# Kernel tuning notes

Hardware: AMD Instinct MI355X
Metric: run time of the kernel (lower is better)

The kernel has to match this reference:

```python
import jax, jax.numpy as jnp
import numpy as np

D_MODEL = 64  # per-head dim used in the scale sqrt(d_model*2)
B, H, S, D = 4, 16, 2048, 64


def setup_inputs() -> dict:
    key = jax.random.key(0)
    kq, kk, kv, kd, ke, km = jax.random.split(key, 6)
    return {
        "Q": jax.random.normal(kq, (B, H, S, D), dtype=jnp.float32),
        "K": jax.random.normal(kk, (B, H, S, D), dtype=jnp.float32),
        "V": jax.random.normal(kv, (B, H, S, D), dtype=jnp.float32),
        "distance_matrix": jax.random.uniform(kd, (B, S, S), dtype=jnp.float32),
        "energy_matrix": jax.random.uniform(ke, (B, S, S), dtype=jnp.float32),
        "mask": jax.random.randint(km, (B, 1, S, S), 0, 2, dtype=jnp.int32),
    }


def reference(Q, K, V, distance_matrix, energy_matrix, mask):
    # distance_matrix and energy_matrix are unused by the original forward.
    scale = 1.0 / np.sqrt(D_MODEL * 2).astype(np.float32)
    scores = jnp.einsum("bhqd,bhkd->bhqk", Q, K) * scale  # [B,H,S,S]
    scores = jnp.where(mask == 0, jnp.float32(-1e9), scores)
    attn = jax.nn.softmax(scores, axis=-1)
    context = jnp.einsum("bhqk,bhkd->bhqd", attn, V)  # [B,H,S,D]
    return context
```

## Files before the change

kernel.cpp:

```cpp
#include <hip/hip_runtime.h>
#include <stdint.h>

#define DEVINL __device__ __forceinline__

typedef float f32x4 __attribute__((ext_vector_type(4)));
typedef float f32x2 __attribute__((ext_vector_type(2)));
typedef short s16x8 __attribute__((ext_vector_type(8)));
typedef short s16x4 __attribute__((ext_vector_type(4)));
typedef unsigned int u32x4 __attribute__((ext_vector_type(4)));

constexpr int Bb = 4, Hh = 16, Ss = 2048, Dd = 64;
constexpr float SCALE = 0.088388347648318447f;
constexpr float QSC = 0.088388347648318447f * 1.4426950408889634f;

DEVINL short f2bf(float x) {
  union { float f; unsigned u; } c; c.f = x;
  unsigned r = (c.u + 0x7fffu + ((c.u >> 16) & 1u)) >> 16;
  return (short)r;
}

DEVINL unsigned pkbf(float a, float b) {
  unsigned r;
  asm("v_cvt_pk_bf16_f32 %0, %1, %2" : "=v"(r) : "v"(a), "v"(b));
  return r;
}

DEVINL void gload_lds16(const short* g, short* l) {
  __builtin_amdgcn_global_load_lds(
      (const __attribute__((address_space(1))) void*)g,
      (__attribute__((address_space(3))) void*)l, 16, 0, 0);
}

__global__ void mask_to_bits(const int* __restrict__ mask,
                             unsigned long long* __restrict__ bits, int n) {
  int gid = blockIdx.x * blockDim.x + threadIdx.x;
  int stride = gridDim.x * blockDim.x;
  for (int i = gid; i < n; i += stride) {
    unsigned long long bal = __ballot(mask[i] != 0);
    if ((i & 63) == 0) bits[i >> 6] = bal;
  }
}

__global__ void kvconv(const float* __restrict__ K, const float* __restrict__ V,
                       short* __restrict__ Kimg, short* __restrict__ Vimg) {
  const int x = blockIdx.x;
  const int sel = x & 1;
  const int t = (x >> 1) & 31;
  const int bh = x >> 6;
  const int tid = threadIdx.x;
  if (sel == 0) {
    const float* Kp = K + ((size_t)bh * Ss + t * 64) * Dd;
    short* img = Kimg + ((size_t)bh * 32 + t) * 4096;
#pragma unroll
    for (int it = 0; it < 4; ++it) {
      int idx = tid + it * 256;
      int kv = idx >> 4, c = idx & 15;
      const float* kr = Kp + (size_t)kv * Dd;
      s16x4 sv;
      sv[0] = f2bf(kr[c]);
      sv[1] = f2bf(kr[c + 16]);
      sv[2] = f2bf(kr[c + 32]);
      sv[3] = f2bf(kr[c + 48]);
      *(s16x4*)(img + kv * 64 + ((4 * c) ^ ((kv & 7) << 3))) = sv;
    }
  } else {
    const float* Vp = V + ((size_t)bh * Ss + t * 64) * Dd;
    short* img = Vimg + ((size_t)bh * 32 + t) * 4096;
    const int d = tid & 63, c4 = tid >> 6;
#pragma unroll
    for (int it = 0; it < 4; ++it) {
      int c = c4 * 4 + it;
      s16x4 sv;
      sv[0] = f2bf(Vp[(size_t)(c) * Dd + d]);
      sv[1] = f2bf(Vp[(size_t)(c + 16) * Dd + d]);
      sv[2] = f2bf(Vp[(size_t)(c + 32) * Dd + d]);
      sv[3] = f2bf(Vp[(size_t)(c + 48) * Dd + d]);
      *(s16x4*)(img + d * 64 + ((4 * c) ^ ((d & 7) << 3))) = sv;
    }
  }
}

__launch_bounds__(256, 5)
__global__ void attn2(const float* __restrict__ Q,
                      const unsigned long long* __restrict__ mbits,
                      const short* __restrict__ Kimg,
                      const short* __restrict__ Vimg,
                      float* __restrict__ Out) {
  __shared__ short lds[16384];

  const int tid = threadIdx.x;
  const int lane = tid & 63;
  const int w = tid >> 6;
  const int l15 = lane & 15;
  const int lq = lane >> 4;

  const int nb = ((blockIdx.x & 7) << 8) | (blockIdx.x >> 3);
  const int qt = nb & 31;
  const int bh = nb >> 5;
  const int b = bh >> 4;

  const float* Qp = Q + (size_t)bh * Ss * Dd;
  float* Op = Out + (size_t)bh * Ss * Dd;
  const short* Kt = Kimg + (size_t)bh * 32 * 4096;
  const short* Vt = Vimg + (size_t)bh * 32 * 4096;
  const int qbW = qt * 64 + w * 16;

  s16x8 qf[2];
  {
    const float* qrow = Qp + (size_t)(qbW + l15) * Dd;
#pragma unroll
    for (int dh = 0; dh < 2; ++dh) {
      s16x8 f;
#pragma unroll
      for (int g = 0; g < 4; ++g) {
        f32x2 v = *(const f32x2*)(qrow + 16 * g + 4 * lq + 2 * dh);
        f[g] = f2bf(v[0] * QSC);
        f[g + 4] = f2bf(v[1] * QSC);
      }
      qf[dh] = f;
    }
  }

  s16x8 onesA;
  {
    short o = (l15 == 0) ? (short)0x3F80 : (short)0;
#pragma unroll
    for (int j = 0; j < 8; ++j) onesA[j] = o;
  }

  f32x4 oacc[4];
  f32x4 lacc = f32x4{0.f, 0.f, 0.f, 0.f};
#pragma unroll
  for (int ds = 0; ds < 4; ++ds) oacc[ds] = f32x4{0.f, 0.f, 0.f, 0.f};

  int off[4][2];
#pragma unroll
  for (int sub = 0; sub < 4; ++sub) {
    int row = sub * 16 + l15;
    int sw = (row & 7) << 3;
    off[sub][0] = row * 64 + ((16 * lq) ^ sw);
    off[sub][1] = row * 64 + ((16 * lq + 8) ^ sw);
  }

  const unsigned long long* mbq = mbits + (size_t)(b * Ss + qbW + l15) * 32;

  auto stage = [&](int buf, int t) {
    short* Lb = lds + buf * 8192;
    const short* gk = Kt + t * 4096 + w * 512 + lane * 8;
    const short* gv = Vt + t * 4096 + w * 512 + lane * 8;
    gload_lds16(gk, Lb + w * 512);
    gload_lds16(gk + 2048, Lb + 2048 + w * 512);
    gload_lds16(gv, Lb + 4096 + w * 512);
    gload_lds16(gv + 2048, Lb + 6144 + w * 512);
  };

  stage(0, 0);

  for (int t = 0; t < 32; ++t) {
    const int cur = t & 1;
    unsigned long long mw = mbq[t];
    __syncthreads();
    if (t < 31) stage(cur ^ 1, t + 1);

    const short* kb = lds + cur * 8192;
    const short* vb = kb + 4096;

    f32x4 bias[4];
    {
      const unsigned mlo = ~(unsigned)(mw >> (4 * lq));
      const unsigned mhi = ~(unsigned)(mw >> (32 + 4 * lq));
#pragma unroll
      for (int sub = 0; sub < 4; ++sub) {
        const unsigned wsrc = (sub < 2) ? mlo : mhi;
        const int base = 16 * (sub & 1);
#pragma unroll
        for (int r = 0; r < 4; ++r) {
          int sb = ((int)(wsrc << (31 - (base + r)))) >> 31;
          bias[sub][r] = __uint_as_float((unsigned)sb & 0xCE6E6B28u);
        }
      }
    }

    f32x4 sc[4];
    __builtin_amdgcn_s_setprio(1);
#pragma unroll
    for (int sub = 0; sub < 4; ++sub) {
      s16x8 k0 = *(const s16x8*)(kb + off[sub][0]);
      s16x8 k1 = *(const s16x8*)(kb + off[sub][1]);
      f32x4 a = bias[sub];
      a = __builtin_amdgcn_mfma_f32_16x16x32_bf16(k0, qf[0], a, 0, 0, 0);
      a = __builtin_amdgcn_mfma_f32_16x16x32_bf16(k1, qf[1], a, 0, 0, 0);
      sc[sub] = a;
    }
    __builtin_amdgcn_s_setprio(0);

    s16x8 pf[2];
#pragma unroll
    for (int sub = 0; sub < 4; ++sub) {
      f32x4 s = sc[sub];
#pragma unroll
      for (int r = 0; r < 4; ++r) s[r] = __builtin_amdgcn_exp2f(s[r]);
      sc[sub] = s;
    }
#pragma unroll
    for (int kvh = 0; kvh < 2; ++kvh) {
      u32x4 wv;
      wv[0] = pkbf(sc[0][2 * kvh], sc[1][2 * kvh]);
      wv[1] = pkbf(sc[2][2 * kvh], sc[3][2 * kvh]);
      wv[2] = pkbf(sc[0][2 * kvh + 1], sc[1][2 * kvh + 1]);
      wv[3] = pkbf(sc[2][2 * kvh + 1], sc[3][2 * kvh + 1]);
      pf[kvh] = __builtin_bit_cast(s16x8, wv);
    }

    __builtin_amdgcn_s_setprio(1);
#pragma unroll
    for (int ds = 0; ds < 4; ++ds) {
      s16x8 v0 = *(const s16x8*)(vb + off[ds][0]);
      s16x8 v1 = *(const s16x8*)(vb + off[ds][1]);
      f32x4 a = oacc[ds];
      a = __builtin_amdgcn_mfma_f32_16x16x32_bf16(v0, pf[0], a, 0, 0, 0);
      a = __builtin_amdgcn_mfma_f32_16x16x32_bf16(v1, pf[1], a, 0, 0, 0);
      oacc[ds] = a;
    }
    lacc = __builtin_amdgcn_mfma_f32_16x16x32_bf16(onesA, pf[0], lacc, 0, 0, 0);
    lacc = __builtin_amdgcn_mfma_f32_16x16x32_bf16(onesA, pf[1], lacc, 0, 0, 0);
    __builtin_amdgcn_s_setprio(0);
  }

  {
    float l = __shfl(lacc[0], l15);
    float inv = 1.f / l;
    float* orow = Op + (size_t)(qbW + l15) * Dd;
#pragma unroll
    for (int ds = 0; ds < 4; ++ds) {
      f32x4 v = oacc[ds];
      v *= inv;
      *(f32x4*)(orow + ds * 16 + 4 * lq) = v;
    }
  }
}

template<bool USEBITS>
__launch_bounds__(256, 2)
__global__ void attn_fwd(const float* __restrict__ Q, const float* __restrict__ K,
                         const float* __restrict__ V, const int* __restrict__ mask,
                         const unsigned long long* __restrict__ mbits,
                         float* __restrict__ Out) {
  __shared__ short Ks[64 * 64];
  __shared__ short Vs[64 * 64];

  const int tid = threadIdx.x;
  const int lane = tid & 63;
  const int w = tid >> 6;
  const int l15 = lane & 15;
  const int lq = lane >> 4;

  const int bid = blockIdx.x;
  const int h = bid & 15;
  const int qt = (bid >> 4) & 7;
  const int b = bid >> 7;

  const int bh = b * Hh + h;
  const float* Qp = Q + (size_t)bh * Ss * Dd;
  const float* Kp = K + (size_t)bh * Ss * Dd;
  const float* Vp = V + (size_t)bh * Ss * Dd;
  float* Op = Out + (size_t)bh * Ss * Dd;

  const int qbW = qt * 256 + w * 64;

  s16x8 qf[4][2];
#pragma unroll
  for (int qs = 0; qs < 4; ++qs) {
    const float* qrow = Qp + (size_t)(qbW + qs * 16 + l15) * Dd;
#pragma unroll
    for (int dh = 0; dh < 2; ++dh) {
      s16x8 f;
#pragma unroll
      for (int g = 0; g < 4; ++g) {
        f32x2 v = *(const f32x2*)(qrow + 16 * g + 4 * lq + 2 * dh);
        f[g] = f2bf(v[0]);
        f[g + 4] = f2bf(v[1]);
      }
      qf[qs][dh] = f;
    }
  }

  f32x4 oacc[4][4];
  float mrun[4], lrun[4];
#pragma unroll
  for (int qs = 0; qs < 4; ++qs) {
    mrun[qs] = -1e30f;
    lrun[qs] = 0.f;
#pragma unroll
    for (int ds = 0; ds < 4; ++ds) oacc[qs][ds] = f32x4{0.f, 0.f, 0.f, 0.f};
  }

  for (int kv0 = 0; kv0 < Ss; kv0 += 64) {
    __syncthreads();
#pragma unroll
    for (int p = 0; p < 4; ++p) {
      int f = tid + p * 256;
      int kv = f >> 4;
      int c = f & 15;
      const float* krow = Kp + (size_t)(kv0 + kv) * Dd;
      s16x4 sv;
      sv[0] = f2bf(krow[c]);
      sv[1] = f2bf(krow[c + 16]);
      sv[2] = f2bf(krow[c + 32]);
      sv[3] = f2bf(krow[c + 48]);
      *(s16x4*)(Ks + kv * 64 + ((4 * c) ^ ((kv & 7) << 3))) = sv;
    }
#pragma unroll
    for (int p = 0; p < 4; ++p) {
      int f = tid + p * 256;
      int kv = f >> 4;
      int c = f & 15;
      f32x4 v = *(const f32x4*)(Vp + (size_t)(kv0 + kv) * Dd + 4 * c);
      int pv = (kv & 15) * 4 + (kv >> 4);
#pragma unroll
      for (int i = 0; i < 4; ++i) {
        int d = 4 * c + i;
        Vs[d * 64 + (pv ^ ((d & 7) << 3))] = f2bf(v[i]);
      }
    }
    __syncthreads();

    s16x8 kf[4][2];
#pragma unroll
    for (int sub = 0; sub < 4; ++sub) {
      int row = sub * 16 + l15;
      const short* base = Ks + row * 64;
      int sw = (row & 7) << 3;
      kf[sub][0] = *(const s16x8*)(base + ((16 * lq + 0) ^ sw));
      kf[sub][1] = *(const s16x8*)(base + ((16 * lq + 8) ^ sw));
    }
    s16x8 vf[4][2];
#pragma unroll
    for (int ds = 0; ds < 4; ++ds) {
      int row = ds * 16 + l15;
      const short* base = Vs + row * 64;
      int sw = (row & 7) << 3;
      vf[ds][0] = *(const s16x8*)(base + ((16 * lq + 0) ^ sw));
      vf[ds][1] = *(const s16x8*)(base + ((16 * lq + 8) ^ sw));
    }

    const int kvw = kv0 >> 6;
#pragma unroll
    for (int qs = 0; qs < 4; ++qs) {
      f32x4 sc[4];
#pragma unroll
      for (int sub = 0; sub < 4; ++sub) {
        f32x4 a = f32x4{0.f, 0.f, 0.f, 0.f};
        a = __builtin_amdgcn_mfma_f32_16x16x32_bf16(kf[sub][0], qf[qs][0], a, 0, 0, 0);
        a = __builtin_amdgcn_mfma_f32_16x16x32_bf16(kf[sub][1], qf[qs][1], a, 0, 0, 0);
        sc[sub] = a;
      }

      const int q = qbW + qs * 16 + l15;
      unsigned long long mw = 0;
      if constexpr (USEBITS) mw = mbits[(size_t)(b * Ss + q) * 32 + kvw];

      float tm = -3e38f;
#pragma unroll
      for (int sub = 0; sub < 4; ++sub) {
        f32x4 s = sc[sub];
        if constexpr (USEBITS) {
          unsigned nib = (unsigned)((mw >> (16 * sub + 4 * lq)) & 0xFULL);
#pragma unroll
          for (int r = 0; r < 4; ++r) {
            float sv = s[r] * SCALE;
            sv = ((nib >> r) & 1u) ? sv : -1e9f;
            s[r] = sv;
            tm = fmaxf(tm, sv);
          }
        } else {
          const int* mrow = mask + ((size_t)b * Ss + q) * Ss + kv0 + 16 * sub + 4 * lq;
          int4 mi = *(const int4*)mrow;
          int mv[4] = {mi.x, mi.y, mi.z, mi.w};
#pragma unroll
          for (int r = 0; r < 4; ++r) {
            float sv = s[r] * SCALE;
            sv = mv[r] ? sv : -1e9f;
            s[r] = sv;
            tm = fmaxf(tm, sv);
          }
        }
        sc[sub] = s;
      }
      tm = fmaxf(tm, __shfl_xor(tm, 16));
      tm = fmaxf(tm, __shfl_xor(tm, 32));
      float mnew = fmaxf(mrun[qs], tm);
      float corr = __expf(mrun[qs] - mnew);
      mrun[qs] = mnew;

      float ps = 0.f;
#pragma unroll
      for (int sub = 0; sub < 4; ++sub) {
        f32x4 s = sc[sub];
#pragma unroll
        for (int r = 0; r < 4; ++r) {
          float p = __expf(s[r] - mnew);
          s[r] = p;
          ps += p;
        }
        sc[sub] = s;
      }
      ps += __shfl_xor(ps, 16);
      ps += __shfl_xor(ps, 32);
      lrun[qs] = lrun[qs] * corr + ps;
#pragma unroll
      for (int ds = 0; ds < 4; ++ds) oacc[qs][ds] *= corr;

      s16x8 pf[2];
#pragma unroll
      for (int kvh = 0; kvh < 2; ++kvh) {
        s16x8 f;
#pragma unroll
        for (int j = 0; j < 8; ++j) f[j] = f2bf(sc[j & 3][2 * kvh + (j >> 2)]);
        pf[kvh] = f;
      }
#pragma unroll
      for (int ds = 0; ds < 4; ++ds) {
        f32x4 a = oacc[qs][ds];
        a = __builtin_amdgcn_mfma_f32_16x16x32_bf16(vf[ds][0], pf[0], a, 0, 0, 0);
        a = __builtin_amdgcn_mfma_f32_16x16x32_bf16(vf[ds][1], pf[1], a, 0, 0, 0);
        oacc[qs][ds] = a;
      }
    }
  }

#pragma unroll
  for (int qs = 0; qs < 4; ++qs) {
    float inv = 1.f / lrun[qs];
    float* orow = Op + (size_t)(qbW + qs * 16 + l15) * Dd;
#pragma unroll
    for (int ds = 0; ds < 4; ++ds) {
      f32x4 v = oacc[qs][ds];
      v *= inv;
      *(f32x4*)(orow + ds * 16 + 4 * lq) = v;
    }
  }
}

extern "C" void kernel_launch(void* const* d_in, const int* in_sizes, int n_in,
                              void* d_out, int out_size, void* d_ws, size_t ws_size,
                              hipStream_t stream) {
  const float* Q = (const float*)d_in[0];
  const float* K = (const float*)d_in[1];
  const float* V = (const float*)d_in[2];
  const int* mask = (const int*)d_in[5];
  float* out = (float*)d_out;

  const int nmask = Bb * Ss * Ss;
  const size_t bitsB = (size_t)(nmask / 64) * 8;
  const size_t imgB = (size_t)Bb * Hh * 32 * 4096 * 2;
  const size_t need = bitsB + 2 * imgB;

  if (d_ws && ws_size >= need) {
    unsigned long long* bits = (unsigned long long*)d_ws;
    short* Kimg = (short*)((char*)d_ws + bitsB);
    short* Vimg = (short*)((char*)d_ws + bitsB + imgB);
    mask_to_bits<<<2048, 256, 0, stream>>>(mask, bits, nmask);
    kvconv<<<Bb * Hh * 32 * 2, 256, 0, stream>>>(K, V, Kimg, Vimg);
    attn2<<<Bb * Hh * (Ss / 64), 256, 0, stream>>>(Q, bits, Kimg, Vimg, out);
  } else if (d_ws && ws_size >= bitsB) {
    unsigned long long* bits = (unsigned long long*)d_ws;
    mask_to_bits<<<2048, 256, 0, stream>>>(mask, bits, nmask);
    attn_fwd<true><<<Bb * Hh * (Ss / 256), 256, 0, stream>>>(Q, K, V, mask, bits, out);
  } else {
    attn_fwd<false><<<Bb * Hh * (Ss / 256), 256, 0, stream>>>(Q, K, V, mask, nullptr, out);
  }
}
```

Before: 144.0 us.

## Process four 16-row query subtiles per wave to reuse K/V LDS fragments

```diff
diff --git a/kernel.cpp b/kernel.cpp
--- a/kernel.cpp
+++ b/kernel.cpp
@@ -80,7 +80,7 @@
   }
 }
 
-__launch_bounds__(256, 5)
+__launch_bounds__(256, 2)
 __global__ void attn2(const float* __restrict__ Q,
                       const unsigned long long* __restrict__ mbits,
                       const short* __restrict__ Kimg,
@@ -94,20 +94,21 @@
   const int l15 = lane & 15;
   const int lq = lane >> 4;
 
-  const int nb = ((blockIdx.x & 7) << 8) | (blockIdx.x >> 3);
-  const int qt = nb & 31;
-  const int bh = nb >> 5;
+  const int nb = ((blockIdx.x & 7) << 6) | (blockIdx.x >> 3);
+  const int qt = nb & 7;
+  const int bh = nb >> 3;
   const int b = bh >> 4;
 
   const float* Qp = Q + (size_t)bh * Ss * Dd;
   float* Op = Out + (size_t)bh * Ss * Dd;
   const short* Kt = Kimg + (size_t)bh * 32 * 4096;
   const short* Vt = Vimg + (size_t)bh * 32 * 4096;
-  const int qbW = qt * 64 + w * 16;
-
-  s16x8 qf[2];
-  {
-    const float* qrow = Qp + (size_t)(qbW + l15) * Dd;
+  const int qbW = qt * 256 + w * 64;
+
+  s16x8 qf[4][2];
+#pragma unroll
+  for (int qs = 0; qs < 4; ++qs) {
+    const float* qrow = Qp + (size_t)(qbW + qs * 16 + l15) * Dd;
 #pragma unroll
     for (int dh = 0; dh < 2; ++dh) {
       s16x8 f;
@@ -117,7 +118,7 @@
         f[g] = f2bf(v[0] * QSC);
         f[g + 4] = f2bf(v[1] * QSC);
       }
-      qf[dh] = f;
+      qf[qs][dh] = f;
     }
   }
 
@@ -128,10 +129,14 @@
     for (int j = 0; j < 8; ++j) onesA[j] = o;
   }
 
-  f32x4 oacc[4];
-  f32x4 lacc = f32x4{0.f, 0.f, 0.f, 0.f};
-#pragma unroll
-  for (int ds = 0; ds < 4; ++ds) oacc[ds] = f32x4{0.f, 0.f, 0.f, 0.f};
+  f32x4 oacc[4][4];
+  f32x4 lacc[4];
+#pragma unroll
+  for (int qs = 0; qs < 4; ++qs) {
+    lacc[qs] = f32x4{0.f, 0.f, 0.f, 0.f};
+#pragma unroll
+    for (int ds = 0; ds < 4; ++ds) oacc[qs][ds] = f32x4{0.f, 0.f, 0.f, 0.f};
+  }
 
   int off[4][2];
 #pragma unroll
@@ -158,82 +163,87 @@
 
   for (int t = 0; t < 32; ++t) {
     const int cur = t & 1;
-    unsigned long long mw = mbq[t];
+    unsigned long long mw[4];
+#pragma unroll
+    for (int qs = 0; qs < 4; ++qs) mw[qs] = mbq[qs * 512 + t];
+
     __syncthreads();
     if (t < 31) stage(cur ^ 1, t + 1);
 
     const short* kb = lds + cur * 8192;
     const short* vb = kb + 4096;
 
-    f32x4 bias[4];
-    {
-      const unsigned mlo = ~(unsigned)(mw >> (4 * lq));
-      const unsigned mhi = ~(unsigned)(mw >> (32 + 4 * lq));
+    s16x8 kf[4][2], vf[4][2];
+#pragma unroll
+    for (int sub = 0; sub < 4; ++sub) {
+      kf[sub][0] = *(const s16x8*)(kb + off[sub][0]);
+      kf[sub][1] = *(const s16x8*)(kb + off[sub][1]);
+      vf[sub][0] = *(const s16x8*)(vb + off[sub][0]);
+      vf[sub][1] = *(const s16x8*)(vb + off[sub][1]);
+    }
+
+#pragma unroll
+    for (int qs = 0; qs < 4; ++qs) {
+      f32x4 sc[4];
+      {
+        const unsigned mlo = ~(unsigned)(mw[qs] >> (4 * lq));
+        const unsigned mhi = ~(unsigned)(mw[qs] >> (32 + 4 * lq));
+#pragma unroll
+        for (int sub = 0; sub < 4; ++sub) {
+          const unsigned wsrc = (sub < 2) ? mlo : mhi;
+          const int base = 16 * (sub & 1);
+#pragma unroll
+          for (int r = 0; r < 4; ++r) {
+            int sb = ((int)(wsrc << (31 - (base + r)))) >> 31;
+            sc[sub][r] = __uint_as_float((unsigned)sb & 0xCE6E6B28u);
+          }
+        }
+      }
+      __builtin_amdgcn_s_setprio(1);
 #pragma unroll
       for (int sub = 0; sub < 4; ++sub) {
-        const unsigned wsrc = (sub < 2) ? mlo : mhi;
-        const int base = 16 * (sub & 1);
-#pragma unroll
-        for (int r = 0; r < 4; ++r) {
-          int sb = ((int)(wsrc << (31 - (base + r)))) >> 31;
-          bias[sub][r] = __uint_as_float((unsigned)sb & 0xCE6E6B28u);
-        }
-      }
-    }
-
-    f32x4 sc[4];
-    __builtin_amdgcn_s_setprio(1);
-#pragma unroll
-    for (int sub = 0; sub < 4; ++sub) {
-      s16x8 k0 = *(const s16x8*)(kb + off[sub][0]);
-      s16x8 k1 = *(const s16x8*)(kb + off[sub][1]);
-      f32x4 a = bias[sub];
-      a = __builtin_amdgcn_mfma_f32_16x16x32_bf16(k0, qf[0], a, 0, 0, 0);
-      a = __builtin_amdgcn_mfma_f32_16x16x32_bf16(k1, qf[1], a, 0, 0, 0);
-      sc[sub] = a;
-    }
-    __builtin_amdgcn_s_setprio(0);
-
-    s16x8 pf[2];
-#pragma unroll
-    for (int sub = 0; sub < 4; ++sub) {
-      f32x4 s = sc[sub];
-#pragma unroll
-      for (int r = 0; r < 4; ++r) s[r] = __builtin_amdgcn_exp2f(s[r]);
-      sc[sub] = s;
-    }
-#pragma unroll
-    for (int kvh = 0; kvh < 2; ++kvh) {
-      u32x4 wv;
-      wv[0] = pkbf(sc[0][2 * kvh], sc[1][2 * kvh]);
-      wv[1] = pkbf(sc[2][2 * kvh], sc[3][2 * kvh]);
-      wv[2] = pkbf(sc[0][2 * kvh + 1], sc[1][2 * kvh + 1]);
-      wv[3] = pkbf(sc[2][2 * kvh + 1], sc[3][2 * kvh + 1]);
-      pf[kvh] = __builtin_bit_cast(s16x8, wv);
-    }
-
-    __builtin_amdgcn_s_setprio(1);
+        sc[sub] = __builtin_amdgcn_mfma_f32_16x16x32_bf16(kf[sub][0], qf[qs][0], sc[sub], 0, 0, 0);
+        sc[sub] = __builtin_amdgcn_mfma_f32_16x16x32_bf16(kf[sub][1], qf[qs][1], sc[sub], 0, 0, 0);
+      }
+      __builtin_amdgcn_s_setprio(0);
+#pragma unroll
+      for (int sub = 0; sub < 4; ++sub) {
+        f32x4 s = sc[sub];
+#pragma unroll
+        for (int r = 0; r < 4; ++r) s[r] = __builtin_amdgcn_exp2f(s[r]);
+        sc[sub] = s;
+      }
+      s16x8 pf[2];
+#pragma unroll
+      for (int kvh = 0; kvh < 2; ++kvh) {
+        u32x4 wv;
+        wv[0] = pkbf(sc[0][2 * kvh], sc[1][2 * kvh]);
+        wv[1] = pkbf(sc[2][2 * kvh], sc[3][2 * kvh]);
+        wv[2] = pkbf(sc[0][2 * kvh + 1], sc[1][2 * kvh + 1]);
+        wv[3] = pkbf(sc[2][2 * kvh + 1], sc[3][2 * kvh + 1]);
+        pf[kvh] = __builtin_bit_cast(s16x8, wv);
+      }
+      __builtin_amdgcn_s_setprio(1);
+#pragma unroll
+      for (int ds = 0; ds < 4; ++ds) {
+        f32x4 a = oacc[qs][ds];
+        a = __builtin_amdgcn_mfma_f32_16x16x32_bf16(vf[ds][0], pf[0], a, 0, 0, 0);
+        oacc[qs][ds] = __builtin_amdgcn_mfma_f32_16x16x32_bf16(vf[ds][1], pf[1], a, 0, 0, 0);
+      }
+      lacc[qs] = __builtin_amdgcn_mfma_f32_16x16x32_bf16(onesA, pf[0], lacc[qs], 0, 0, 0);
+      lacc[qs] = __builtin_amdgcn_mfma_f32_16x16x32_bf16(onesA, pf[1], lacc[qs], 0, 0, 0);
+      __builtin_amdgcn_s_setprio(0);
+    }
+  }
+
+#pragma unroll
+  for (int qs = 0; qs < 4; ++qs) {
+    float l = __shfl(lacc[qs][0], l15);
+    float inv = 1.f / l;
+    float* orow = Op + (size_t)(qbW + qs * 16 + l15) * Dd;
 #pragma unroll
     for (int ds = 0; ds < 4; ++ds) {
-      s16x8 v0 = *(const s16x8*)(vb + off[ds][0]);
-      s16x8 v1 = *(const s16x8*)(vb + off[ds][1]);
-      f32x4 a = oacc[ds];
-      a = __builtin_amdgcn_mfma_f32_16x16x32_bf16(v0, pf[0], a, 0, 0, 0);
-      a = __builtin_amdgcn_mfma_f32_16x16x32_bf16(v1, pf[1], a, 0, 0, 0);
-      oacc[ds] = a;
-    }
-    lacc = __builtin_amdgcn_mfma_f32_16x16x32_bf16(onesA, pf[0], lacc, 0, 0, 0);
-    lacc = __builtin_amdgcn_mfma_f32_16x16x32_bf16(onesA, pf[1], lacc, 0, 0, 0);
-    __builtin_amdgcn_s_setprio(0);
-  }
-
-  {
-    float l = __shfl(lacc[0], l15);
-    float inv = 1.f / l;
-    float* orow = Op + (size_t)(qbW + l15) * Dd;
-#pragma unroll
-    for (int ds = 0; ds < 4; ++ds) {
-      f32x4 v = oacc[ds];
+      f32x4 v = oacc[qs][ds];
       v *= inv;
       *(f32x4*)(orow + ds * 16 + 4 * lq) = v;
     }
@@ -462,7 +472,7 @@
     short* Vimg = (short*)((char*)d_ws + bitsB + imgB);
     mask_to_bits<<<2048, 256, 0, stream>>>(mask, bits, nmask);
     kvconv<<<Bb * Hh * 32 * 2, 256, 0, stream>>>(K, V, Kimg, Vimg);
-    attn2<<<Bb * Hh * (Ss / 64), 256, 0, stream>>>(Q, bits, Kimg, Vimg, out);
+    attn2<<<512, 256, 0, stream>>>(Q, bits, Kimg, Vimg, out);
   } else if (d_ws && ws_size >= bitsB) {
     unsigned long long* bits = (unsigned long long*)d_ws;
     mask_to_bits<<<2048, 256, 0, stream>>>(mask, bits, nmask);
```

Measured after the change: 142.3 us. No clear change (-1.2%).
